# Kernel optimization log

Hardware: AMD Instinct MI355X
Metric: run time of the kernel (lower is better)

The kernel has to match this reference:

```python
import jax, jax.numpy as jnp
import numpy as np

B, T, D = 2, 2048, 1024
N_HEADS = 16
HEAD_DIM = D // N_HEADS
HIDDEN = 4 * D
LN_EPS = 1e-6  # flax LayerNorm default


def apply_rotary_pos_emb(x, positions):
    # x: (B, T, H, head_dim); positions: (T,)
    head_dim = x.shape[-1]
    inv_freq = 1.0 / 10000 ** (jnp.arange(0, head_dim, 2).astype(jnp.float32) / head_dim)
    freqs = jnp.outer(positions.astype(jnp.float32), inv_freq)  # (T, head_dim//2)
    cos_emb = jnp.cos(freqs)[None, :, None, :]
    sin_emb = jnp.sin(freqs)[None, :, None, :]
    x1 = x[..., : head_dim // 2]
    x2 = x[..., head_dim // 2 :]
    return jnp.concatenate([x1 * cos_emb - x2 * sin_emb,
                            x1 * sin_emb + x2 * cos_emb], axis=-1)


def layernorm(x, scale, bias):
    mu = jnp.mean(x, axis=-1, keepdims=True)
    var = jnp.mean(jnp.square(x - mu), axis=-1, keepdims=True)
    return (x - mu) * jax.lax.rsqrt(var + LN_EPS) * scale + bias


def setup_inputs() -> dict:
    key = jax.random.key(0)
    ks = jax.random.split(key, 8)
    lecun = lambda k, shape: jax.random.normal(k, shape, jnp.float32) * (1.0 / np.sqrt(shape[0]))
    x = jax.random.normal(ks[0], (B, T, D), jnp.float32)
    positions = jnp.arange(T, dtype=jnp.int32)
    mask = jnp.tril(jnp.ones((T, T), dtype=bool))[None, None]  # causal (1,1,T,T)
    return {
        "x": x,
        "positions": positions,
        "mask": mask,
        "ln1_scale": jnp.ones((D,), jnp.float32),
        "ln1_bias": jnp.zeros((D,), jnp.float32),
        "w_qkv": lecun(ks[1], (D, 3 * D)),
        "w_o": lecun(ks[2], (D, D)),
        "ln2_scale": jnp.ones((D,), jnp.float32),
        "ln2_bias": jnp.zeros((D,), jnp.float32),
        "w1": lecun(ks[3], (D, HIDDEN)),
        "b1": jnp.zeros((HIDDEN,), jnp.float32),
        "w2": lecun(ks[4], (HIDDEN, D)),
        "b2": jnp.zeros((D,), jnp.float32),
    }


def reference(x, positions, mask, ln1_scale, ln1_bias, w_qkv, w_o,
              ln2_scale, ln2_bias, w1, b1, w2, b2):
    h = layernorm(x, ln1_scale, ln1_bias)
    qkv = h @ w_qkv  # (B,T,3D)
    qkv = qkv.reshape(B, T, 3, N_HEADS, HEAD_DIM)
    q, k, v = jnp.moveaxis(qkv, 2, 0)  # each (B,T,H,hd)
    q = apply_rotary_pos_emb(q, positions)
    k = apply_rotary_pos_emb(k, positions)
    q = jnp.transpose(q, (0, 2, 1, 3))  # (B,H,T,hd)
    k = jnp.transpose(k, (0, 2, 1, 3))
    v = jnp.transpose(v, (0, 2, 1, 3))
    scale = 1.0 / jnp.sqrt(jnp.float32(HEAD_DIM))
    attn_weights = jnp.einsum('bhqd,bhkd->bhqk', q, k) * scale
    attn_weights = jnp.where(mask, attn_weights, -1e10)
    attn_weights = jax.nn.softmax(attn_weights, axis=-1)
    h = jnp.einsum('bhqk,bhkd->bhqd', attn_weights, v)
    h = jnp.transpose(h, (0, 2, 1, 3)).reshape(B, T, D)
    h = h @ w_o
    x = x + h
    h = layernorm(x, ln2_scale, ln2_bias)
    h = jax.nn.gelu(h @ w1 + b1)  # approximate gelu, matching flax nn.gelu default
    h = h @ w2 + b2
    return x + h
```

## Files before the change

kernel.cpp:

```cpp
#include <hip/hip_runtime.h>


typedef __bf16 bf16_t;
typedef bf16_t bf16x8 __attribute__((ext_vector_type(8)));
typedef float f32x4 __attribute__((ext_vector_type(4)));

#define M_ROWS 4096
#define DMODEL 1024
#define TSEQ   2048
#define NHEAD  16
#define HDIM   64

__device__ __forceinline__ ushort f2bf(float f) {
  union { float f; unsigned u; } v; v.f = f;
  unsigned r = (v.u + 0x7fffu + ((v.u >> 16) & 1u)) >> 16;
  return (ushort)r;
}
__device__ __forceinline__ float bf2f(ushort u) {
  union { unsigned u; float f; } v; v.u = ((unsigned)u) << 16;
  return v.f;
}
__device__ __forceinline__ unsigned cvt_pk_bf16(float a, float b) {
  unsigned r;
  asm("v_cvt_pk_bf16_f32 %0, %1, %2" : "=v"(r) : "v"(a), "v"(b));
  return r;
}
__device__ __forceinline__ void gload_lds16(const void* g, void* l) {
  __builtin_amdgcn_global_load_lds(
      (const __attribute__((address_space(1))) unsigned*)g,
      (__attribute__((address_space(3))) unsigned*)l, 16, 0, 0);
}
__device__ __forceinline__ f32x4 mfma16(bf16x8 a, bf16x8 b, f32x4 c) {
  return __builtin_amdgcn_mfma_f32_16x16x32_bf16(a, b, c, 0, 0, 0);
}
__device__ __forceinline__ float gelu_f(float x) {
  float y = 0.7978845608028654f * (x + 0.044715f * x * x * x);
  float e = __expf(2.0f * y);
  float t = 1.0f - 2.0f / (e + 1.0f);
  return 0.5f * x * (1.0f + t);
}

__global__ __launch_bounds__(256)
void transpose_all(const float* __restrict__ wqkv, const float* __restrict__ wo,
                   const float* __restrict__ w1, const float* __restrict__ w2,
                   ushort* __restrict__ dqkv, ushort* __restrict__ dwo,
                   ushort* __restrict__ dw1, ushort* __restrict__ dw2) {
  int id = blockIdx.x;
  const float* src; ushort* dst; int K, N, nx, loc;
  if (id < 3072)      { src = wqkv; dst = dqkv; K = 1024; N = 3072; nx = 96;  loc = id; }
  else if (id < 4096) { src = wo;   dst = dwo;  K = 1024; N = 1024; nx = 32;  loc = id - 3072; }
  else if (id < 8192) { src = w1;   dst = dw1;  K = 1024; N = 4096; nx = 128; loc = id - 4096; }
  else                { src = w2;   dst = dw2;  K = 4096; N = 1024; nx = 32;  loc = id - 8192; }
  int n0 = (loc % nx) * 32, k0 = (loc / nx) * 32;
  __shared__ float t[32][33];
  int tx = threadIdx.x & 31, ty = threadIdx.x >> 5;
#pragma unroll
  for (int i = 0; i < 4; i++) {
    int k = ty + i * 8;
    t[k][tx] = src[(size_t)(k0 + k) * N + n0 + tx];
  }
  __syncthreads();
#pragma unroll
  for (int i = 0; i < 4; i++) {
    int nn = ty + i * 8;
    dst[(size_t)(n0 + nn) * K + k0 + tx] = f2bf(t[tx][nn]);
  }
}

__global__ __launch_bounds__(256)
void ln_kernel(const float* __restrict__ x, const float* __restrict__ sc,
               const float* __restrict__ bi, ushort* __restrict__ out) {
  int row = blockIdx.x;
  int tid = threadIdx.x;
  const float4 v = *(const float4*)&x[(size_t)row * DMODEL + tid * 4];
  float s = v.x + v.y + v.z + v.w;
  float s2 = v.x * v.x + v.y * v.y + v.z * v.z + v.w * v.w;
#pragma unroll
  for (int off = 32; off > 0; off >>= 1) {
    s += __shfl_down(s, off);
    s2 += __shfl_down(s2, off);
  }
  __shared__ float red[8];
  int lane = tid & 63, w = tid >> 6;
  if (lane == 0) { red[w * 2] = s; red[w * 2 + 1] = s2; }
  __syncthreads();
  float S = red[0] + red[2] + red[4] + red[6];
  float S2 = red[1] + red[3] + red[5] + red[7];
  float mu = S * (1.0f / DMODEL);
  float var = S2 * (1.0f / DMODEL) - mu * mu;
  float rs = rsqrtf(var + 1e-6f);
  float4 scv = *(const float4*)&sc[tid * 4];
  float4 biv = *(const float4*)&bi[tid * 4];
  ushort4 o;
  o.x = f2bf((v.x - mu) * rs * scv.x + biv.x);
  o.y = f2bf((v.y - mu) * rs * scv.y + biv.y);
  o.z = f2bf((v.z - mu) * rs * scv.z + biv.z);
  o.w = f2bf((v.w - mu) * rs * scv.w + biv.w);
  *(ushort4*)&out[(size_t)row * DMODEL + tid * 4] = o;
}

__global__ __launch_bounds__(256)
void rope_table(const int* __restrict__ positions, float2* __restrict__ tab) {
  int i = blockIdx.x * 256 + threadIdx.x;
  int t = i >> 5, f = i & 31;
  float inv = __expf(-(float)f * (1.0f / 32.0f) * 9.210340371976184f);
  float a = (float)positions[t] * inv;
  tab[i] = make_float2(cosf(a), sinf(a));
}

__global__ __launch_bounds__(256)
void qkv_gemm(const ushort* __restrict__ A, const ushort* __restrict__ Bt,
              const float2* __restrict__ tab, ushort* __restrict__ Qo,
              ushort* __restrict__ Ko, ushort* __restrict__ VTo, int K,
              int nbn) {
  constexpr int NF = 2;
  __shared__ char smem[49152];
  ushort* lA = (ushort*)smem;
  ushort* lB = (ushort*)(smem + 32768);
  int tid = threadIdx.x;
  int lane = tid & 63, w = tid >> 6;
  int wm = w >> 1, wn = w & 1;

  int nwg = gridDim.x;
  int cpx = nwg >> 3;
  int wg = ((int)blockIdx.x & 7) * cpx + ((int)blockIdx.x >> 3);
  int bm = wg / nbn, bn = wg % nbn;

  f32x4 acc[4][NF] = {};

  const ushort* Ab = A + (size_t)bm * 128 * K;
  const ushort* Bb = Bt + (size_t)bn * 64 * K;
  int lrow = lane & 15, lg = lane >> 4;
  int srow = tid >> 3, sch = tid & 7;

  auto stage = [&](int buf, int k0) {
#pragma unroll
    for (int c = 0; c < 4; c++) {
      int r = c * 32 + srow;
      int gch = sch ^ (r & 7);
      gload_lds16(Ab + (size_t)r * K + k0 + gch * 8,
                  &lA[buf * 8192 + c * 2048 + tid * 8]);
    }
#pragma unroll
    for (int c = 0; c < 2; c++) {
      int r = c * 32 + srow;
      int gch = sch ^ (r & 7);
      gload_lds16(Bb + (size_t)r * K + k0 + gch * 8,
                  &lB[buf * 4096 + c * 2048 + tid * 8]);
    }
  };

  int nt = K >> 6;
  stage(0, 0);
  __syncthreads();

  for (int t = 0; t < nt; ++t) {
    int cur = t & 1;
    bf16x8 af0[4], af1[4], bf0[NF], bf1[NF];
#pragma unroll
    for (int m = 0; m < 4; m++) {
      int row = wm * 64 + m * 16 + lrow;
      const ushort* p = &lA[cur * 8192 + row * 64];
      af0[m] = *(const bf16x8*)(p + (((lg    ) ^ (row & 7)) << 3));
      af1[m] = *(const bf16x8*)(p + (((lg + 4) ^ (row & 7)) << 3));
    }
#pragma unroll
    for (int n = 0; n < NF; n++) {
      int row = wn * 32 + n * 16 + lrow;
      const ushort* p = &lB[cur * 4096 + row * 64];
      bf0[n] = *(const bf16x8*)(p + (((lg    ) ^ (row & 7)) << 3));
      bf1[n] = *(const bf16x8*)(p + (((lg + 4) ^ (row & 7)) << 3));
    }
    if (t + 1 < nt) stage(cur ^ 1, (t + 1) << 6);
    __builtin_amdgcn_s_setprio(1);
#pragma unroll
    for (int m = 0; m < 4; m++)
#pragma unroll
      for (int n = 0; n < NF; n++)
        acc[m][n] = mfma16(af0[m], bf0[n], acc[m][n]);
#pragma unroll
    for (int m = 0; m < 4; m++)
#pragma unroll
      for (int n = 0; n < NF; n++)
        acc[m][n] = mfma16(af1[m], bf1[n], acc[m][n]);
    __builtin_amdgcn_s_setprio(0);
    __builtin_amdgcn_sched_barrier(0);
    asm volatile("s_waitcnt vmcnt(0)" ::: "memory");
    __builtin_amdgcn_s_barrier();
  }

  float* lt = (float*)smem;
#pragma unroll
  for (int m = 0; m < 4; m++) {
    int row = wm * 64 + m * 16 + lg * 4;
#pragma unroll
    for (int n = 0; n < NF; n++) {
      int col = wn * 32 + n * 16 + lrow;
#pragma unroll
      for (int r = 0; r < 4; r++)
        lt[(row + r) * 68 + col] = acc[m][n][r];
    }
  }
  __syncthreads();

  int t0 = bm * 128;
  int b = t0 >> 11;
  int tloc = t0 & 2047;

  if (bn < 32) {
    bool isQ = (bn < 16);
    int h = bn & 15;
    const float QS = 0.125f * 1.44269504088896340736f;
    float sc = isQ ? QS : 1.0f;
    ushort* dst = (isQ ? Qo : Ko) + ((size_t)(b * NHEAD + h) * TSEQ) * HDIM;
    int row = tid >> 1, f0 = (tid & 1) * 16;
    int t = tloc + row;
    ushort lo[16], hi[16];
#pragma unroll
    for (int j = 0; j < 16; j++) {
      int f = f0 + j;
      float2 cs = tab[t * 32 + f];
      float x1 = lt[row * 68 + f], x2 = lt[row * 68 + f + 32];
      lo[j] = f2bf((x1 * cs.x - x2 * cs.y) * sc);
      hi[j] = f2bf((x1 * cs.y + x2 * cs.x) * sc);
    }
    ushort* dr = dst + (size_t)t * HDIM;
#pragma unroll
    for (int c = 0; c < 4; c++) {
      *(ushort4*)&dr[f0 + c * 4]      = *(ushort4*)&lo[c * 4];
      *(ushort4*)&dr[32 + f0 + c * 4] = *(ushort4*)&hi[c * 4];
    }
  } else {
    int h = bn - 32;
    ushort* dst = VTo + (size_t)(b * NHEAD + h) * HDIM * TSEQ;
    int f = tid >> 2, tc0 = (tid & 3) * 32;
    ushort buf[32];
#pragma unroll
    for (int j = 0; j < 32; j++)
      buf[j] = f2bf(lt[(tc0 + j) * 68 + f]);
    ushort* dr = dst + (size_t)f * TSEQ + tloc + tc0;
#pragma unroll
    for (int c = 0; c < 8; c++)
      *(ushort4*)&dr[c * 4] = *(ushort4*)&buf[c * 4];
  }
}

__global__ __launch_bounds__(256, 4)
void attn_kernel(const ushort* __restrict__ Q, const ushort* __restrict__ Kd,
                 const ushort* __restrict__ VT, ushort* __restrict__ O) {
  int bh = blockIdx.x;
  int p = blockIdx.y;
  int tid = threadIdx.x;
  int lane = tid & 63, w = tid >> 6;
  int lr = lane & 15, lg = lane >> 4;

  const ushort* Qb = Q + (size_t)bh * TSEQ * HDIM;
  const ushort* Kb = Kd + (size_t)bh * TSEQ * HDIM;
  const ushort* Vb = VT + (size_t)bh * HDIM * TSEQ;

  __shared__ ushort lK[2][64 * 64];
  __shared__ ushort lV[2][64 * 64];
  __shared__ ushort pt[4][16 * 64];
  ushort* myp = pt[w];

  int srow0 = tid >> 3, sch = tid & 7;

  auto stage = [&](int buf, int kt) {
#pragma unroll
    for (int c = 0; c < 2; c++) {
      int r = c * 32 + srow0;
      int gch = sch ^ (r & 7);
      gload_lds16(Kb + (size_t)(kt + r) * HDIM + gch * 8,
                  &lK[buf][c * 2048 + tid * 8]);
      gload_lds16(Vb + (size_t)r * TSEQ + kt + gch * 8,
                  &lV[buf][c * 2048 + tid * 8]);
    }
  };

  int b = bh >> 4, h = bh & 15;

  for (int half = 0; half < 2; half++) {
    int qb = half == 0 ? (31 - p) : p;
    int nt = qb + 1;
    int qw = qb * 64 + w * 16;
    int q_abs = qw + lr;

    bf16x8 aq0 = *(const bf16x8*)&Qb[(size_t)q_abs * HDIM + lg * 8];
    bf16x8 aq1 = *(const bf16x8*)&Qb[(size_t)q_abs * HDIM + 32 + lg * 8];

    float m_run = -1e30f, l_run = 0.0f;
    f32x4 o[4] = {};

    stage(0, 0);
    __syncthreads();

    for (int it = 0; it < nt; ++it) {
      int kt = it * 64;
      int buf = it & 1;
      bool diag = (it == nt - 1);

      if (it + 1 < nt) stage(buf ^ 1, kt + 64);

      f32x4 sa[4];
#pragma unroll
      for (int cb = 0; cb < 4; cb++) {
        int row = cb * 16 + lr;
        const ushort* kp = &lK[buf][row * 64];
        bf16x8 k0 = *(const bf16x8*)(kp + (((lg    ) ^ (row & 7)) << 3));
        bf16x8 k1 = *(const bf16x8*)(kp + (((lg + 4) ^ (row & 7)) << 3));
        f32x4 z = {};
        z = mfma16(k0, aq0, z);
        sa[cb] = mfma16(k1, aq1, z);
      }

      if (diag) {
#pragma unroll
        for (int cb = 0; cb < 4; cb++)
#pragma unroll
          for (int r = 0; r < 4; r++)
            if (kt + cb * 16 + lg * 4 + r > q_abs) sa[cb][r] = -1e30f;
      }

      f32x4 m4;
#pragma unroll
      for (int r = 0; r < 4; r++)
        m4[r] = fmaxf(fmaxf(sa[0][r], sa[1][r]), fmaxf(sa[2][r], sa[3][r]));
      float mx = fmaxf(fmaxf(m4[0], m4[1]), fmaxf(m4[2], m4[3]));
      mx = fmaxf(mx, __shfl_xor(mx, 16, 64));
      mx = fmaxf(mx, __shfl_xor(mx, 32, 64));
      float mn = fmaxf(m_run, mx);
      float rescale = __builtin_amdgcn_exp2f(m_run - mn);
      m_run = mn;

      float ps = 0.0f;
      uint2 pk[4];
#pragma unroll
      for (int cb = 0; cb < 4; cb++) {
        float p0 = __builtin_amdgcn_exp2f(sa[cb][0] - mn);
        float p1 = __builtin_amdgcn_exp2f(sa[cb][1] - mn);
        float p2 = __builtin_amdgcn_exp2f(sa[cb][2] - mn);
        float p3 = __builtin_amdgcn_exp2f(sa[cb][3] - mn);
        ps += (p0 + p1) + (p2 + p3);
        pk[cb].x = cvt_pk_bf16(p0, p1);
        pk[cb].y = cvt_pk_bf16(p2, p3);
      }
      ps += __shfl_xor(ps, 16, 64);
      ps += __shfl_xor(ps, 32, 64);
      l_run = l_run * rescale + ps;

#pragma unroll
      for (int cb = 0; cb < 4; cb++)
        *(uint2*)&myp[lr * 64 + (((cb * 4 + lg) ^ lr) << 2)] = pk[cb];

#pragma unroll
      for (int d = 0; d < 4; d++)
#pragma unroll
        for (int r = 0; r < 4; r++) o[d][r] *= rescale;

      union U8 { uint2 h[2]; bf16x8 v; };
      U8 t0, t1;
      t0.h[0] = *(const uint2*)&myp[lr * 64 + (((lg * 2    ) ^ lr) << 2)];
      t0.h[1] = *(const uint2*)&myp[lr * 64 + (((lg * 2 + 1) ^ lr) << 2)];
      t1.h[0] = *(const uint2*)&myp[lr * 64 + (((8 + lg * 2    ) ^ lr) << 2)];
      t1.h[1] = *(const uint2*)&myp[lr * 64 + (((8 + lg * 2 + 1) ^ lr) << 2)];

#pragma unroll
      for (int d = 0; d < 4; d++) {
        int row = d * 16 + lr;
        const ushort* vp = &lV[buf][row * 64];
        bf16x8 va0 = *(const bf16x8*)(vp + (((lg    ) ^ (row & 7)) << 3));
        bf16x8 va1 = *(const bf16x8*)(vp + (((lg + 4) ^ (row & 7)) << 3));
        o[d] = mfma16(va0, t0.v, o[d]);
        o[d] = mfma16(va1, t1.v, o[d]);
      }

      __syncthreads();
    }

    float linv = 1.0f / l_run;
    size_t obase = (size_t)(b * TSEQ + qw + lr) * DMODEL + h * 64;
#pragma unroll
    for (int d = 0; d < 4; d++) {
      uint2 st;
      st.x = cvt_pk_bf16(o[d][0] * linv, o[d][1] * linv);
      st.y = cvt_pk_bf16(o[d][2] * linv, o[d][3] * linv);
      *(uint2*)&O[obase + d * 16 + lg * 4] = st;
    }
  }
}

template <int EPI, int BN>
__global__ __launch_bounds__(256)
void gemm_kernel(const ushort* __restrict__ A, const ushort* __restrict__ Bt,
                 void* __restrict__ Cout, const float* __restrict__ bias,
                 const float* __restrict__ resid, int M, int N, int K,
                 int nbn) {
  constexpr int NF = BN / 32;
  __shared__ ushort lA[2][128 * 64];
  __shared__ ushort lB[2][BN * 64];
  int tid = threadIdx.x;
  int lane = tid & 63, w = tid >> 6;
  int wm = w >> 1, wn = w & 1;

  int nwg = gridDim.x;
  int cpx = nwg >> 3;
  int wg = ((int)blockIdx.x & 7) * cpx + ((int)blockIdx.x >> 3);
  int bm = wg / nbn, bn = wg % nbn;

  f32x4 acc[4][NF] = {};

  const ushort* Ab = A + (size_t)bm * 128 * K;
  const ushort* Bb = Bt + (size_t)bn * BN * K;
  int lrow = lane & 15, lg = lane >> 4;
  int srow = tid >> 3, sch = tid & 7;

  auto stage = [&](int buf, int k0) {
#pragma unroll
    for (int c = 0; c < 4; c++) {
      int r = c * 32 + srow;
      int gch = sch ^ (r & 7);
      gload_lds16(Ab + (size_t)r * K + k0 + gch * 8,
                  &lA[buf][c * 2048 + tid * 8]);
    }
#pragma unroll
    for (int c = 0; c < NF; c++) {
      int r = c * 32 + srow;
      int gch = sch ^ (r & 7);
      gload_lds16(Bb + (size_t)r * K + k0 + gch * 8,
                  &lB[buf][c * 2048 + tid * 8]);
    }
  };

  int nt = K >> 6;
  stage(0, 0);
  __syncthreads();

  for (int t = 0; t < nt; ++t) {
    int cur = t & 1;

    bf16x8 af0[4], af1[4], bf0[NF], bf1[NF];
#pragma unroll
    for (int m = 0; m < 4; m++) {
      int row = wm * 64 + m * 16 + lrow;
      const ushort* p = &lA[cur][row * 64];
      af0[m] = *(const bf16x8*)(p + (((lg    ) ^ (row & 7)) << 3));
      af1[m] = *(const bf16x8*)(p + (((lg + 4) ^ (row & 7)) << 3));
    }
#pragma unroll
    for (int n = 0; n < NF; n++) {
      int row = wn * (BN / 2) + n * 16 + lrow;
      const ushort* p = &lB[cur][row * 64];
      bf0[n] = *(const bf16x8*)(p + (((lg    ) ^ (row & 7)) << 3));
      bf1[n] = *(const bf16x8*)(p + (((lg + 4) ^ (row & 7)) << 3));
    }

    if (t + 1 < nt) stage(cur ^ 1, (t + 1) << 6);

    __builtin_amdgcn_s_setprio(1);
#pragma unroll
    for (int m = 0; m < 4; m++)
#pragma unroll
      for (int n = 0; n < NF; n++)
        acc[m][n] = mfma16(af0[m], bf0[n], acc[m][n]);
#pragma unroll
    for (int m = 0; m < 4; m++)
#pragma unroll
      for (int n = 0; n < NF; n++)
        acc[m][n] = mfma16(af1[m], bf1[n], acc[m][n]);
    __builtin_amdgcn_s_setprio(0);

    __builtin_amdgcn_sched_barrier(0);
    asm volatile("s_waitcnt vmcnt(0)" ::: "memory");
    __builtin_amdgcn_s_barrier();
  }

#pragma unroll
  for (int m = 0; m < 4; m++) {
    int rbase = bm * 128 + wm * 64 + m * 16 + (lane >> 4) * 4;
#pragma unroll
    for (int n = 0; n < NF; n++) {
      int c = bn * BN + wn * (BN / 2) + n * 16 + (lane & 15);
#pragma unroll
      for (int r = 0; r < 4; r++) {
        float v = acc[m][n][r];
        size_t idx = (size_t)(rbase + r) * N + c;
        if constexpr (EPI == 0) {
          ((ushort*)Cout)[idx] = f2bf(v);
        } else if constexpr (EPI == 1) {
          ((float*)Cout)[idx] = v + resid[idx];
        } else if constexpr (EPI == 2) {
          ((ushort*)Cout)[idx] = f2bf(gelu_f(v + bias[c]));
        } else {
          ((float*)Cout)[idx] = v + bias[c] + resid[idx];
        }
      }
    }
  }
}

extern "C" void kernel_launch(void* const* d_in, const int* in_sizes, int n_in,
                              void* d_out, int out_size, void* d_ws,
                              size_t ws_size, hipStream_t stream) {
  const float* x      = (const float*)d_in[0];
  const int* positions = (const int*)d_in[1];
  const float* ln1_s  = (const float*)d_in[3];
  const float* ln1_b  = (const float*)d_in[4];
  const float* w_qkv  = (const float*)d_in[5];
  const float* w_o    = (const float*)d_in[6];
  const float* ln2_s  = (const float*)d_in[7];
  const float* ln2_b  = (const float*)d_in[8];
  const float* w1     = (const float*)d_in[9];
  const float* b1     = (const float*)d_in[10];
  const float* w2     = (const float*)d_in[11];
  const float* b2     = (const float*)d_in[12];
  float* out = (float*)d_out;

  char* ws = (char*)d_ws;
  size_t off = 0;
  auto nxt = [&](size_t bytes) {
    char* p = ws + off;
    off += (bytes + 255) & ~(size_t)255;
    return p;
  };
  ushort* wqkvT = (ushort*)nxt(3072ULL * 1024 * 2);
  ushort* woT   = (ushort*)nxt(1024ULL * 1024 * 2);
  ushort* w1T   = (ushort*)nxt(4096ULL * 1024 * 2);
  ushort* w2T   = (ushort*)nxt(1024ULL * 4096 * 2);
  ushort* h1    = (ushort*)nxt((size_t)M_ROWS * DMODEL * 2);
  ushort* Qb    = (ushort*)nxt(2ULL * NHEAD * TSEQ * HDIM * 2);
  ushort* Kb    = (ushort*)nxt(2ULL * NHEAD * TSEQ * HDIM * 2);
  ushort* VTb   = (ushort*)nxt(2ULL * NHEAD * TSEQ * HDIM * 2);
  ushort* attn  = (ushort*)nxt((size_t)M_ROWS * DMODEL * 2);
  float*  x2    = (float*)nxt((size_t)M_ROWS * DMODEL * 4);
  ushort* h2    = (ushort*)nxt((size_t)M_ROWS * DMODEL * 2);
  ushort* mid   = (ushort*)nxt((size_t)M_ROWS * 4096 * 2);
  float2* tab   = (float2*)nxt((size_t)TSEQ * 32 * 8);

  transpose_all<<<12288, 256, 0, stream>>>(w_qkv, w_o, w1, w2,
                                           wqkvT, woT, w1T, w2T);
  rope_table<<<(TSEQ * 32) / 256, 256, 0, stream>>>(positions, tab);
  ln_kernel<<<M_ROWS, 256, 0, stream>>>(x, ln1_s, ln1_b, h1);
  qkv_gemm<<<1536, 256, 0, stream>>>(h1, wqkvT, tab, Qb, Kb, VTb, 1024, 48);
  attn_kernel<<<dim3(32, 16), 256, 0, stream>>>(Qb, Kb, VTb, attn);
  gemm_kernel<1, 64><<<512, 256, 0, stream>>>(attn, woT, x2, nullptr, x, 4096, 1024, 1024, 16);
  ln_kernel<<<M_ROWS, 256, 0, stream>>>(x2, ln2_s, ln2_b, h2);
  gemm_kernel<2, 128><<<1024, 256, 0, stream>>>(h2, w1T, mid, b1, nullptr, 4096, 4096, 1024, 32);
  gemm_kernel<3, 64><<<512, 256, 0, stream>>>(mid, w2T, out, b2, x2, 4096, 1024, 4096, 16);
}
```

Measured before the change: 225.9 us.

## Use triple-buffered LDS pipeline in GEMMs and shrink FFN1 tile to 64

The QKV and generic GEMM kernels move from double-buffered to triple-buffered LDS staging in dynamic shared memory. Loads are issued two tiles ahead, and a partial vmcnt wait plus a single barrier per iteration replaces the full drain at the end of each step. The FFN1 GEMM drops its 128-wide N tile for the shared 64-wide tile and doubles its grid, so all GEMMs use one tile shape. The goal is to hide global load latency behind MFMA work, at the cost of 72KB of LDS per block (lower occupancy) and less B-tile reuse in FFN1.

```diff
diff --git a/kernel.cpp b/kernel.cpp
--- a/kernel.cpp
+++ b/kernel.cpp
@@ -108,15 +108,15 @@
   tab[i] = make_float2(cosf(a), sinf(a));
 }
 
+
 __global__ __launch_bounds__(256)
 void qkv_gemm(const ushort* __restrict__ A, const ushort* __restrict__ Bt,
               const float2* __restrict__ tab, ushort* __restrict__ Qo,
               ushort* __restrict__ Ko, ushort* __restrict__ VTo, int K,
               int nbn) {
-  constexpr int NF = 2;
-  __shared__ char smem[49152];
-  ushort* lA = (ushort*)smem;
-  ushort* lB = (ushort*)(smem + 32768);
+  extern __shared__ ushort smem[];
+  ushort* lA = smem;
+  ushort* lB = smem + 24576;
   int tid = threadIdx.x;
   int lane = tid & 63, w = tid >> 6;
   int wm = w >> 1, wn = w & 1;
@@ -126,7 +126,7 @@
   int wg = ((int)blockIdx.x & 7) * cpx + ((int)blockIdx.x >> 3);
   int bm = wg / nbn, bn = wg % nbn;
 
-  f32x4 acc[4][NF] = {};
+  f32x4 acc[4][2] = {};
 
   const ushort* Ab = A + (size_t)bm * 128 * K;
   const ushort* Bb = Bt + (size_t)bn * 64 * K;
@@ -152,11 +152,18 @@
 
   int nt = K >> 6;
   stage(0, 0);
-  __syncthreads();
-
+  stage(1, 64);
+
+  int cur = 0;
   for (int t = 0; t < nt; ++t) {
-    int cur = t & 1;
-    bf16x8 af0[4], af1[4], bf0[NF], bf1[NF];
+    if (t + 1 < nt) asm volatile("s_waitcnt vmcnt(6)" ::: "memory");
+    else            asm volatile("s_waitcnt vmcnt(0)" ::: "memory");
+    __builtin_amdgcn_s_barrier();
+
+    int nb = cur + 2; if (nb >= 3) nb -= 3;
+    if (t + 2 < nt) stage(nb, (t + 2) << 6);
+
+    bf16x8 af0[4], af1[4], bf0[2], bf1[2];
 #pragma unroll
     for (int m = 0; m < 4; m++) {
       int row = wm * 64 + m * 16 + lrow;
@@ -165,36 +172,33 @@
       af1[m] = *(const bf16x8*)(p + (((lg + 4) ^ (row & 7)) << 3));
     }
 #pragma unroll
-    for (int n = 0; n < NF; n++) {
+    for (int n = 0; n < 2; n++) {
       int row = wn * 32 + n * 16 + lrow;
       const ushort* p = &lB[cur * 4096 + row * 64];
       bf0[n] = *(const bf16x8*)(p + (((lg    ) ^ (row & 7)) << 3));
       bf1[n] = *(const bf16x8*)(p + (((lg + 4) ^ (row & 7)) << 3));
     }
-    if (t + 1 < nt) stage(cur ^ 1, (t + 1) << 6);
+
     __builtin_amdgcn_s_setprio(1);
 #pragma unroll
     for (int m = 0; m < 4; m++)
 #pragma unroll
-      for (int n = 0; n < NF; n++)
+      for (int n = 0; n < 2; n++) {
         acc[m][n] = mfma16(af0[m], bf0[n], acc[m][n]);
-#pragma unroll
-    for (int m = 0; m < 4; m++)
-#pragma unroll
-      for (int n = 0; n < NF; n++)
         acc[m][n] = mfma16(af1[m], bf1[n], acc[m][n]);
+      }
     __builtin_amdgcn_s_setprio(0);
-    __builtin_amdgcn_sched_barrier(0);
-    asm volatile("s_waitcnt vmcnt(0)" ::: "memory");
-    __builtin_amdgcn_s_barrier();
-  }
+
+    cur = (cur + 1 == 3) ? 0 : cur + 1;
+  }
+  __builtin_amdgcn_s_barrier();
 
   float* lt = (float*)smem;
 #pragma unroll
   for (int m = 0; m < 4; m++) {
     int row = wm * 64 + m * 16 + lg * 4;
 #pragma unroll
-    for (int n = 0; n < NF; n++) {
+    for (int n = 0; n < 2; n++) {
       int col = wn * 32 + n * 16 + lrow;
 #pragma unroll
       for (int r = 0; r < 4; r++)
@@ -389,15 +393,15 @@
   }
 }
 
-template <int EPI, int BN>
+template <int EPI>
 __global__ __launch_bounds__(256)
 void gemm_kernel(const ushort* __restrict__ A, const ushort* __restrict__ Bt,
                  void* __restrict__ Cout, const float* __restrict__ bias,
                  const float* __restrict__ resid, int M, int N, int K,
                  int nbn) {
-  constexpr int NF = BN / 32;
-  __shared__ ushort lA[2][128 * 64];
-  __shared__ ushort lB[2][BN * 64];
+  extern __shared__ ushort smem[];
+  ushort* lA = smem;
+  ushort* lB = smem + 24576;
   int tid = threadIdx.x;
   int lane = tid & 63, w = tid >> 6;
   int wm = w >> 1, wn = w & 1;
@@ -407,10 +411,10 @@
   int wg = ((int)blockIdx.x & 7) * cpx + ((int)blockIdx.x >> 3);
   int bm = wg / nbn, bn = wg % nbn;
 
-  f32x4 acc[4][NF] = {};
+  f32x4 acc[4][2] = {};
 
   const ushort* Ab = A + (size_t)bm * 128 * K;
-  const ushort* Bb = Bt + (size_t)bn * BN * K;
+  const ushort* Bb = Bt + (size_t)bn * 64 * K;
   int lrow = lane & 15, lg = lane >> 4;
   int srow = tid >> 3, sch = tid & 7;
 
@@ -420,73 +424,70 @@
       int r = c * 32 + srow;
       int gch = sch ^ (r & 7);
       gload_lds16(Ab + (size_t)r * K + k0 + gch * 8,
-                  &lA[buf][c * 2048 + tid * 8]);
-    }
-#pragma unroll
-    for (int c = 0; c < NF; c++) {
+                  &lA[buf * 8192 + c * 2048 + tid * 8]);
+    }
+#pragma unroll
+    for (int c = 0; c < 2; c++) {
       int r = c * 32 + srow;
       int gch = sch ^ (r & 7);
       gload_lds16(Bb + (size_t)r * K + k0 + gch * 8,
-                  &lB[buf][c * 2048 + tid * 8]);
+                  &lB[buf * 4096 + c * 2048 + tid * 8]);
     }
   };
 
   int nt = K >> 6;
   stage(0, 0);
-  __syncthreads();
-
+  stage(1, 64);
+
+  int cur = 0;
   for (int t = 0; t < nt; ++t) {
-    int cur = t & 1;
-
-    bf16x8 af0[4], af1[4], bf0[NF], bf1[NF];
+    if (t + 1 < nt) asm volatile("s_waitcnt vmcnt(6)" ::: "memory");
+    else            asm volatile("s_waitcnt vmcnt(0)" ::: "memory");
+    __builtin_amdgcn_s_barrier();
+
+    int nb = cur + 2; if (nb >= 3) nb -= 3;
+    if (t + 2 < nt) stage(nb, (t + 2) << 6);
+
+    bf16x8 af0[4], af1[4], bf0[2], bf1[2];
 #pragma unroll
     for (int m = 0; m < 4; m++) {
       int row = wm * 64 + m * 16 + lrow;
-      const ushort* p = &lA[cur][row * 64];
+      const ushort* p = &lA[cur * 8192 + row * 64];
       af0[m] = *(const bf16x8*)(p + (((lg    ) ^ (row & 7)) << 3));
       af1[m] = *(const bf16x8*)(p + (((lg + 4) ^ (row & 7)) << 3));
     }
 #pragma unroll
-    for (int n = 0; n < NF; n++) {
-      int row = wn * (BN / 2) + n * 16 + lrow;
-      const ushort* p = &lB[cur][row * 64];
+    for (int n = 0; n < 2; n++) {
+      int row = wn * 32 + n * 16 + lrow;
+      const ushort* p = &lB[cur * 4096 + row * 64];
       bf0[n] = *(const bf16x8*)(p + (((lg    ) ^ (row & 7)) << 3));
       bf1[n] = *(const bf16x8*)(p + (((lg + 4) ^ (row & 7)) << 3));
     }
 
-    if (t + 1 < nt) stage(cur ^ 1, (t + 1) << 6);
-
     __builtin_amdgcn_s_setprio(1);
 #pragma unroll
     for (int m = 0; m < 4; m++)
 #pragma unroll
-      for (int n = 0; n < NF; n++)
+      for (int n = 0; n < 2; n++) {
         acc[m][n] = mfma16(af0[m], bf0[n], acc[m][n]);
-#pragma unroll
-    for (int m = 0; m < 4; m++)
-#pragma unroll
-      for (int n = 0; n < NF; n++)
         acc[m][n] = mfma16(af1[m], bf1[n], acc[m][n]);
+      }
     __builtin_amdgcn_s_setprio(0);
 
-    __builtin_amdgcn_sched_barrier(0);
-    asm volatile("s_waitcnt vmcnt(0)" ::: "memory");
-    __builtin_amdgcn_s_barrier();
+    cur = (cur + 1 == 3) ? 0 : cur + 1;
   }
 
 #pragma unroll
   for (int m = 0; m < 4; m++) {
     int rbase = bm * 128 + wm * 64 + m * 16 + (lane >> 4) * 4;
 #pragma unroll
-    for (int n = 0; n < NF; n++) {
-      int c = bn * BN + wn * (BN / 2) + n * 16 + (lane & 15);
+    for (int n = 0; n < 2; n++) {
+      int c = bn * 64 + wn * 32 + n * 16 + (lane & 15);
 #pragma unroll
       for (int r = 0; r < 4; r++) {
         float v = acc[m][n][r];
         size_t idx = (size_t)(rbase + r) * N + c;
-        if constexpr (EPI == 0) {
-          ((ushort*)Cout)[idx] = f2bf(v);
-        } else if constexpr (EPI == 1) {
+        if constexpr (EPI == 1) {
           ((float*)Cout)[idx] = v + resid[idx];
         } else if constexpr (EPI == 2) {
           ((ushort*)Cout)[idx] = f2bf(gelu_f(v + bias[c]));
@@ -536,14 +537,23 @@
   ushort* mid   = (ushort*)nxt((size_t)M_ROWS * 4096 * 2);
   float2* tab   = (float2*)nxt((size_t)TSEQ * 32 * 8);
 
+  (void)hipFuncSetAttribute((const void*)qkv_gemm,
+                            hipFuncAttributeMaxDynamicSharedMemorySize, 73728);
+  (void)hipFuncSetAttribute((const void*)gemm_kernel<1>,
+                            hipFuncAttributeMaxDynamicSharedMemorySize, 73728);
+  (void)hipFuncSetAttribute((const void*)gemm_kernel<2>,
+                            hipFuncAttributeMaxDynamicSharedMemorySize, 73728);
+  (void)hipFuncSetAttribute((const void*)gemm_kernel<3>,
+                            hipFuncAttributeMaxDynamicSharedMemorySize, 73728);
+
   transpose_all<<<12288, 256, 0, stream>>>(w_qkv, w_o, w1, w2,
                                            wqkvT, woT, w1T, w2T);
   rope_table<<<(TSEQ * 32) / 256, 256, 0, stream>>>(positions, tab);
   ln_kernel<<<M_ROWS, 256, 0, stream>>>(x, ln1_s, ln1_b, h1);
-  qkv_gemm<<<1536, 256, 0, stream>>>(h1, wqkvT, tab, Qb, Kb, VTb, 1024, 48);
+  qkv_gemm<<<1536, 256, 73728, stream>>>(h1, wqkvT, tab, Qb, Kb, VTb, 1024, 48);
   attn_kernel<<<dim3(32, 16), 256, 0, stream>>>(Qb, Kb, VTb, attn);
-  gemm_kernel<1, 64><<<512, 256, 0, stream>>>(attn, woT, x2, nullptr, x, 4096, 1024, 1024, 16);
+  gemm_kernel<1><<<512, 256, 73728, stream>>>(attn, woT, x2, nullptr, x, 4096, 1024, 1024, 16);
   ln_kernel<<<M_ROWS, 256, 0, stream>>>(x2, ln2_s, ln2_b, h2);
-  gemm_kernel<2, 128><<<1024, 256, 0, stream>>>(h2, w1T, mid, b1, nullptr, 4096, 4096, 1024, 32);
-  gemm_kernel<3, 64><<<512, 256, 0, stream>>>(mid, w2T, out, b2, x2, 4096, 1024, 4096, 16);
-}
+  gemm_kernel<2><<<2048, 256, 73728, stream>>>(h2, w1T, mid, b1, nullptr, 4096, 4096, 1024, 64);
+  gemm_kernel<3><<<512, 256, 73728, stream>>>(mid, w2T, out, b2, x2, 4096, 1024, 4096, 16);
+}
```

After: 229.4 us. About the same (+1.5%).
